# Kernel optimization log

Measured on AMD Instinct MI355X. Metric: run time of the kernel, lower is better.

The kernel has to match this reference:

```python
import jax, jax.numpy as jnp
import numpy as np

B, N, D, K = 16, 4096, 256, 2048  # batch, tokens, dim, codebook_size
COMMIT = 0.25

def setup_inputs() -> dict:
    key = jax.random.key(0)
    k1, k2 = jax.random.split(key)
    x = jax.random.normal(k1, (B, N, D), dtype=jnp.float32)
    # codebook buffer, stored as [dim, codebook_size] like lucidrains' VectorQuantize
    embed = jax.random.normal(k2, (D, K), dtype=jnp.float32)
    return {"x": x, "embed": embed}

def reference(x, embed):
    # flatten tokens: [B*N, D]
    flat = x.reshape(-1, D)
    # squared euclidean distance to every code: [B*N, K]
    dist = (jnp.sum(flat * flat, axis=1, keepdims=True)
            - 2.0 * (flat @ embed)
            + jnp.sum(embed * embed, axis=0, keepdims=True))
    idx = jnp.argmin(dist, axis=1)          # nearest code per token, [B*N]
    indices = idx.reshape(B, N)
    quantize = embed.T[indices]             # gather codes -> [B, N, D]
    # commitment loss: mse(quantize.detach(), x) * commitment
    commit_loss = jnp.mean(jnp.square(jax.lax.stop_gradient(quantize) - x)) * COMMIT
    # straight-through estimator
    quantize = x + jax.lax.stop_gradient(quantize - x)
    return quantize, commit_loss, indices
```

## Files before the change

kernel.cpp:

```cpp
#include <hip/hip_runtime.h>

#define TOK   65536
#define DIMS  256
#define NCODE 2048
#define LOSSOFF 16777216
#define IDXOFF  16777217

typedef _Float16 f16x8 __attribute__((ext_vector_type(8)));
typedef _Float16 f16x4 __attribute__((ext_vector_type(4)));
typedef float    f32x4 __attribute__((ext_vector_type(4)));

__device__ __forceinline__ void ld16(void* lds, const void* g) {
  __builtin_amdgcn_global_load_lds(
      (const __attribute__((address_space(1))) unsigned int*)g,
      (__attribute__((address_space(3))) unsigned int*)lds, 16, 0, 0);
}
__device__ __forceinline__ unsigned long long umin64(unsigned long long a,
                                                     unsigned long long b) {
  return a < b ? a : b;
}

__global__ void k_prep(const float* __restrict__ embed, float* __restrict__ embedT,
                       _Float16* __restrict__ eTh, _Float16* __restrict__ eTl) {
  __shared__ float t[32][33];
  int tx = threadIdx.x & 31, ty = threadIdx.x >> 5;
  int k0 = blockIdx.x * 32, d0 = blockIdx.y * 32;
#pragma unroll
  for (int i = 0; i < 4; ++i) {
    int d = ty + i * 8;
    t[tx][d] = embed[(size_t)(d0 + d) * NCODE + k0 + tx];
  }
  __syncthreads();
#pragma unroll
  for (int i = 0; i < 4; ++i) {
    int kl = ty + i * 8;
    float v = t[kl][tx];
    size_t o = (size_t)(k0 + kl) * DIMS + d0 + tx;
    embedT[o] = v;
    _Float16 h = (_Float16)v;
    eTh[o] = h;
    eTl[o] = (_Float16)(v - (float)h);
  }
}

__global__ void k_e2(const float* __restrict__ embed, float* __restrict__ e2) {
  int k = blockIdx.x * 256 + threadIdx.x;
  double a = 0.0;
  for (int d = 0; d < DIMS; ++d) {
    float v = embed[(size_t)d * NCODE + k];
    a += (double)v * (double)v;
  }
  e2[k] = (float)a;
}

__global__ void k_xsplit(const float* __restrict__ x, _Float16* __restrict__ xh,
                         _Float16* __restrict__ xl,
                         unsigned long long* __restrict__ part,
                         float* __restrict__ out) {
  int gid = blockIdx.x * 256 + threadIdx.x;
  if (gid < TOK) part[gid] = ~0ull;
  if (gid == 0) out[LOSSOFF] = 0.0f;
  size_t base = (size_t)gid;
#pragma unroll
  for (int i = 0; i < 8; ++i) {
    size_t o = (base + (size_t)i * 524288) * 4;
    f32x4 v = *(const f32x4*)&x[o];
    f16x4 h, l;
#pragma unroll
    for (int e = 0; e < 4; ++e) {
      h[e] = (_Float16)v[e];
      l[e] = (_Float16)(v[e] - (float)h[e]);
    }
    *(f16x4*)&xh[o] = h;
    *(f16x4*)&xl[o] = l;
  }
}

#define MM(ah_, al_, bh_, bl_, a_) do { \
  a_ = __builtin_amdgcn_mfma_f32_16x16x32_f16(ah_, bh_, a_, 0, 0, 0); \
  a_ = __builtin_amdgcn_mfma_f32_16x16x32_f16(ah_, bl_, a_, 0, 0, 0); \
  a_ = __builtin_amdgcn_mfma_f32_16x16x32_f16(al_, bh_, a_, 0, 0, 0); } while (0)

__global__ __launch_bounds__(512, 1) void k_score(
    const _Float16* __restrict__ xh, const _Float16* __restrict__ xl,
    const _Float16* __restrict__ eTh, const _Float16* __restrict__ eTl,
    const float* __restrict__ e2, unsigned long long* __restrict__ part) {
  __shared__ __attribute__((aligned(16))) _Float16 Ah[3][256 * 32];
  __shared__ __attribute__((aligned(16))) _Float16 Al[3][256 * 32];
  __shared__ __attribute__((aligned(16))) _Float16 Bh[3][128 * 32];
  __shared__ __attribute__((aligned(16))) _Float16 Bl[3][128 * 32];

  int tid = threadIdx.x, lane = tid & 63, wid = tid >> 6;
  int wm = wid >> 1, wn = wid & 1;
  int bid = blockIdx.x;
  int wg = (bid & 7) * 512 + (bid >> 3);
  int mblk = wg >> 4, nblk = wg & 15;
  int t0 = mblk * 256, c0 = nblk * 128;
  int col = lane & 15, kg = lane >> 4;

  f32x4 acc[4][4] = {};

  auto stageA = [&](int ck, int slot) {
    int kb = ck * 32;
#pragma unroll
    for (int q = 0; q < 2; ++q) {
      int i = q * 512 + wid * 64 + lane;
      int row = i >> 2;
      int g = (i & 3) ^ ((row >> 1) & 3);
      size_t src = (size_t)(t0 + row) * DIMS + kb + g * 8;
      ld16(&Ah[slot][(q * 512 + wid * 64) * 8], &xh[src]);
      ld16(&Al[slot][(q * 512 + wid * 64) * 8], &xl[src]);
    }
  };
  auto stageB = [&](int ck, int slot) {
    int kb = ck * 32;
    int i = wid * 64 + lane;
    int row = i >> 2;
    int g = (i & 3) ^ ((row >> 1) & 3);
    size_t src = (size_t)(c0 + row) * DIMS + kb + g * 8;
    ld16(&Bh[slot][(wid * 64) * 8], &eTh[src]);
    ld16(&Bl[slot][(wid * 64) * 8], &eTl[src]);
  };
  auto rdA = [&](int slot, int mf, f16x8& h, f16x8& l) {
    int row = wm * 64 + mf * 16 + col;
    int off = row * 32 + (kg ^ ((row >> 1) & 3)) * 8;
    h = *(const f16x8*)&Ah[slot][off];
    l = *(const f16x8*)&Al[slot][off];
  };
  auto rdB = [&](int slot, int nf, f16x8& h, f16x8& l) {
    int row = wn * 64 + nf * 16 + col;
    int off = row * 32 + (kg ^ ((row >> 1) & 3)) * 8;
    h = *(const f16x8*)&Bh[slot][off];
    l = *(const f16x8*)&Bl[slot][off];
  };

  stageA(0, 0); stageB(0, 0);
  stageA(1, 1); stageB(1, 1);
  asm volatile("s_waitcnt vmcnt(6)" ::: "memory");
  __builtin_amdgcn_sched_barrier(0);
  __builtin_amdgcn_s_barrier();
  __builtin_amdgcn_sched_barrier(0);

#pragma unroll
  for (int c = 0; c < 8; ++c) {
    int slot = c % 3;
    f16x8 ah[4], al[4], bh[4], bl[4];
#pragma unroll
    for (int m = 0; m < 4; ++m) rdA(slot, m, ah[m], al[m]);
#pragma unroll
    for (int n = 0; n < 4; ++n) rdB(slot, n, bh[n], bl[n]);
    __builtin_amdgcn_sched_barrier(0);
    if (c < 6) { stageA(c + 2, (c + 2) % 3); stageB(c + 2, (c + 2) % 3); }
    __builtin_amdgcn_sched_barrier(0);
    __builtin_amdgcn_s_setprio(1);
#pragma unroll
    for (int m = 0; m < 4; ++m)
#pragma unroll
      for (int n = 0; n < 4; ++n)
        MM(ah[m], al[m], bh[n], bl[n], acc[m][n]);
    __builtin_amdgcn_s_setprio(0);
    __builtin_amdgcn_sched_barrier(0);
    if (c < 6) {
      asm volatile("s_waitcnt vmcnt(6)" ::: "memory");
    } else if (c == 6) {
      asm volatile("s_waitcnt vmcnt(0)" ::: "memory");
    }
    __builtin_amdgcn_sched_barrier(0);
    if (c < 7) __builtin_amdgcn_s_barrier();
    __builtin_amdgcn_sched_barrier(0);
  }

  float e2n[4];
#pragma unroll
  for (int n = 0; n < 4; ++n) e2n[n] = e2[c0 + wn * 64 + n * 16 + col];
#pragma unroll
  for (int m = 0; m < 4; ++m)
#pragma unroll
    for (int r = 0; r < 4; ++r) {
      unsigned long long best = ~0ull;
#pragma unroll
      for (int n = 0; n < 4; ++n) {
        float s = e2n[n] - 2.0f * acc[m][n][r];
        unsigned u = __float_as_uint(s);
        u ^= (u & 0x80000000u) ? 0xFFFFFFFFu : 0x80000000u;
        best = umin64(best, ((unsigned long long)u << 32) |
                            (unsigned)(c0 + wn * 64 + n * 16 + col));
      }
#pragma unroll
      for (int off = 1; off < 16; off <<= 1)
        best = umin64(best, __shfl_xor(best, off, 64));
      if (col == 0)
        atomicMin(&part[t0 + wm * 64 + m * 16 + kg * 4 + r], best);
    }
}

__global__ void k_gather(const float* __restrict__ x, const float* __restrict__ embedT,
                         const unsigned long long* __restrict__ part,
                         float* __restrict__ out) {
  int wid = threadIdx.x >> 6, lane = threadIdx.x & 63;
  int gw = blockIdx.x * 4 + wid;
  float s = 0.0f;
#pragma unroll
  for (int t = 0; t < 8; ++t) {
    int token = gw * 8 + t;
    int code = (int)(part[token] & 0xFFFFFFFFull);
    if (lane == 0) out[IDXOFF + token] = (float)code;
    f32x4 q  = *(const f32x4*)&embedT[(size_t)code * DIMS + lane * 4];
    f32x4 xv = *(const f32x4*)&x[(size_t)token * DIMS + lane * 4];
    f32x4 d = q - xv;
    *(f32x4*)&out[(size_t)token * DIMS + lane * 4] = xv + d;
    s += d[0] * d[0] + d[1] * d[1] + d[2] * d[2] + d[3] * d[3];
  }
  for (int off = 32; off; off >>= 1) s += __shfl_xor(s, off, 64);
  __shared__ float red[4];
  if (lane == 0) red[wid] = s;
  __syncthreads();
  if (threadIdx.x == 0) {
    float tsum = (red[0] + red[1] + red[2] + red[3]) * (0.25f / 16777216.0f);
    atomicAdd(&out[LOSSOFF], tsum);
  }
}

extern "C" void kernel_launch(void* const* d_in, const int* in_sizes, int n_in,
                              void* d_out, int out_size, void* d_ws, size_t ws_size,
                              hipStream_t stream) {
  const float* x     = (const float*)d_in[0];
  const float* embed = (const float*)d_in[1];
  float* out = (float*)d_out;
  _Float16* xh = (_Float16*)d_out;
  _Float16* xl = (_Float16*)((char*)d_out + (32u << 20));
  char* w = (char*)d_ws;
  _Float16* eTh    = (_Float16*)w;
  _Float16* eTl    = (_Float16*)(w + (1u << 20));
  float*    embedT = (float*)(w + (2u << 20));
  float*    e2     = (float*)(w + (4u << 20));
  unsigned long long* part = (unsigned long long*)(w + (4u << 20) + (1u << 15));

  hipLaunchKernelGGL(k_prep,   dim3(NCODE / 32, DIMS / 32), dim3(256), 0, stream, embed, embedT, eTh, eTl);
  hipLaunchKernelGGL(k_e2,     dim3(NCODE / 256),           dim3(256), 0, stream, embed, e2);
  hipLaunchKernelGGL(k_xsplit, dim3(2048),                  dim3(256), 0, stream, x, xh, xl, part, out);
  hipLaunchKernelGGL(k_score,  dim3(4096),                  dim3(512), 0, stream, xh, xl, eTh, eTl, e2, part);
  hipLaunchKernelGGL(k_gather, dim3(2048),                  dim3(256), 0, stream, x, embedT, part, out);
}
```

Measured before the change: 508.5 us.

## Shrink score tile to 128x128, load codebook directly to registers, double-buffer LDS

The score kernel moves from 512-thread blocks with 256x128 tiles and a triple-buffered LDS pipeline for both operands to 256-thread blocks with 128x128 tiles. Only the token operand is staged in LDS, double-buffered. The codebook operand is read straight from global memory into registers each k-step. The smaller LDS footprint and launch bounds of 3 blocks per CU aim to raise occupancy and hide latency through more resident waves. The cost is halved reuse of codebook data, uncoalesced per-lane global loads of codebook fragments on the critical path, and simpler __syncthreads-based synchronisation in place of the tuned waitcnt scheduling.

Result: slower. 522.4 us (+2.7%).

```diff
diff --git a/kernel.cpp b/kernel.cpp
--- a/kernel.cpp
+++ b/kernel.cpp
@@ -81,92 +81,67 @@
   a_ = __builtin_amdgcn_mfma_f32_16x16x32_f16(ah_, bl_, a_, 0, 0, 0); \
   a_ = __builtin_amdgcn_mfma_f32_16x16x32_f16(al_, bh_, a_, 0, 0, 0); } while (0)
 
-__global__ __launch_bounds__(512, 1) void k_score(
+__global__ __launch_bounds__(256, 3) void k_score(
     const _Float16* __restrict__ xh, const _Float16* __restrict__ xl,
     const _Float16* __restrict__ eTh, const _Float16* __restrict__ eTl,
     const float* __restrict__ e2, unsigned long long* __restrict__ part) {
-  __shared__ __attribute__((aligned(16))) _Float16 Ah[3][256 * 32];
-  __shared__ __attribute__((aligned(16))) _Float16 Al[3][256 * 32];
-  __shared__ __attribute__((aligned(16))) _Float16 Bh[3][128 * 32];
-  __shared__ __attribute__((aligned(16))) _Float16 Bl[3][128 * 32];
+  __shared__ __attribute__((aligned(16))) _Float16 Ah[2][128 * 32];
+  __shared__ __attribute__((aligned(16))) _Float16 Al[2][128 * 32];
 
   int tid = threadIdx.x, lane = tid & 63, wid = tid >> 6;
   int wm = wid >> 1, wn = wid & 1;
   int bid = blockIdx.x;
-  int wg = (bid & 7) * 512 + (bid >> 3);
+  int wg = (bid & 7) * 1024 + (bid >> 3);
   int mblk = wg >> 4, nblk = wg & 15;
-  int t0 = mblk * 256, c0 = nblk * 128;
+  int t0 = mblk * 128, c0 = nblk * 128;
   int col = lane & 15, kg = lane >> 4;
 
   f32x4 acc[4][4] = {};
 
-  auto stageA = [&](int ck, int slot) {
+  auto stage = [&](int ck, int buf) {
     int kb = ck * 32;
 #pragma unroll
     for (int q = 0; q < 2; ++q) {
-      int i = q * 512 + wid * 64 + lane;
-      int row = i >> 2;
-      int g = (i & 3) ^ ((row >> 1) & 3);
-      size_t src = (size_t)(t0 + row) * DIMS + kb + g * 8;
-      ld16(&Ah[slot][(q * 512 + wid * 64) * 8], &xh[src]);
-      ld16(&Al[slot][(q * 512 + wid * 64) * 8], &xl[src]);
+      int i = wid * 2 + q;
+      int row = i * 16 + (lane >> 2);
+      int g = (lane & 3) ^ ((row >> 1) & 3);
+      int src = (t0 + row) * DIMS + kb + g * 8;
+      ld16(&Ah[buf][i * 512], &xh[src]);
+      ld16(&Al[buf][i * 512], &xl[src]);
     }
   };
-  auto stageB = [&](int ck, int slot) {
-    int kb = ck * 32;
-    int i = wid * 64 + lane;
-    int row = i >> 2;
-    int g = (i & 3) ^ ((row >> 1) & 3);
-    size_t src = (size_t)(c0 + row) * DIMS + kb + g * 8;
-    ld16(&Bh[slot][(wid * 64) * 8], &eTh[src]);
-    ld16(&Bl[slot][(wid * 64) * 8], &eTl[src]);
-  };
-  auto rdA = [&](int slot, int mf, f16x8& h, f16x8& l) {
+  auto rdA = [&](int buf, int mf, f16x8& h, f16x8& l) {
     int row = wm * 64 + mf * 16 + col;
     int off = row * 32 + (kg ^ ((row >> 1) & 3)) * 8;
-    h = *(const f16x8*)&Ah[slot][off];
-    l = *(const f16x8*)&Al[slot][off];
+    h = *(const f16x8*)&Ah[buf][off];
+    l = *(const f16x8*)&Al[buf][off];
   };
-  auto rdB = [&](int slot, int nf, f16x8& h, f16x8& l) {
-    int row = wn * 64 + nf * 16 + col;
-    int off = row * 32 + (kg ^ ((row >> 1) & 3)) * 8;
-    h = *(const f16x8*)&Bh[slot][off];
-    l = *(const f16x8*)&Bl[slot][off];
+  auto ldB = [&](int ck, int nf, f16x8& h, f16x8& l) {
+    int off = (c0 + wn * 64 + nf * 16 + col) * DIMS + ck * 32 + kg * 8;
+    h = *(const f16x8*)&eTh[off];
+    l = *(const f16x8*)&eTl[off];
   };
 
-  stageA(0, 0); stageB(0, 0);
-  stageA(1, 1); stageB(1, 1);
-  asm volatile("s_waitcnt vmcnt(6)" ::: "memory");
+  stage(0, 0);
+  __syncthreads();
   __builtin_amdgcn_sched_barrier(0);
-  __builtin_amdgcn_s_barrier();
-  __builtin_amdgcn_sched_barrier(0);
 
 #pragma unroll
   for (int c = 0; c < 8; ++c) {
-    int slot = c % 3;
-    f16x8 ah[4], al[4], bh[4], bl[4];
-#pragma unroll
-    for (int m = 0; m < 4; ++m) rdA(slot, m, ah[m], al[m]);
-#pragma unroll
-    for (int n = 0; n < 4; ++n) rdB(slot, n, bh[n], bl[n]);
-    __builtin_amdgcn_sched_barrier(0);
-    if (c < 6) { stageA(c + 2, (c + 2) % 3); stageB(c + 2, (c + 2) % 3); }
-    __builtin_amdgcn_sched_barrier(0);
-    __builtin_amdgcn_s_setprio(1);
+    int buf = c & 1;
+    if (c < 7) stage(c + 1, buf ^ 1);
+    f16x8 bh[4], bl[4];
+#pragma unroll
+    for (int n = 0; n < 4; ++n) ldB(c, n, bh[n], bl[n]);
+    f16x8 ah[4], al[4];
+#pragma unroll
+    for (int m = 0; m < 4; ++m) rdA(buf, m, ah[m], al[m]);
 #pragma unroll
     for (int m = 0; m < 4; ++m)
 #pragma unroll
       for (int n = 0; n < 4; ++n)
         MM(ah[m], al[m], bh[n], bl[n], acc[m][n]);
-    __builtin_amdgcn_s_setprio(0);
-    __builtin_amdgcn_sched_barrier(0);
-    if (c < 6) {
-      asm volatile("s_waitcnt vmcnt(6)" ::: "memory");
-    } else if (c == 6) {
-      asm volatile("s_waitcnt vmcnt(0)" ::: "memory");
-    }
-    __builtin_amdgcn_sched_barrier(0);
-    if (c < 7) __builtin_amdgcn_s_barrier();
+    __syncthreads();
     __builtin_amdgcn_sched_barrier(0);
   }
 
@@ -239,6 +214,6 @@
   hipLaunchKernelGGL(k_prep,   dim3(NCODE / 32, DIMS / 32), dim3(256), 0, stream, embed, embedT, eTh, eTl);
   hipLaunchKernelGGL(k_e2,     dim3(NCODE / 256),           dim3(256), 0, stream, embed, e2);
   hipLaunchKernelGGL(k_xsplit, dim3(2048),                  dim3(256), 0, stream, x, xh, xl, part, out);
-  hipLaunchKernelGGL(k_score,  dim3(4096),                  dim3(512), 0, stream, xh, xl, eTh, eTl, e2, part);
+  hipLaunchKernelGGL(k_score,  dim3(8192),                  dim3(256), 0, stream, xh, xl, eTh, eTl, e2, part);
   hipLaunchKernelGGL(k_gather, dim3(2048),                  dim3(256), 0, stream, x, embedT, part, out);
 }
```
